# Optimization experiments

Hardware: AMD Instinct MI355X
Metric: run time of the kernel (lower is better)

The kernel has to match this reference:

```python
import jax, jax.numpy as jnp
import numpy as np

EBD_DIM = 32
N_PARTS = 17
B, P, H, W = 16, 20, 128, 128


def _gather_vecs(ebds, kpts):
    # ebds: [17*D, H, W]; kpts: [P, 17, 2] normalized coords in [0,1)
    D = EBD_DIM
    flat = ebds.reshape(N_PARTS, D, H * W).transpose(0, 2, 1)  # [17, HW, D]
    ys = jnp.floor(kpts[..., 0] * H).astype(jnp.int32)          # [P, 17]
    xs = jnp.floor(kpts[..., 1] * W).astype(jnp.int32)          # [P, 17]
    lin = ys * W + xs                                           # [P, 17]
    k = jnp.arange(N_PARTS)[None, :]                            # [1, 17] part index
    return flat[k, lin]                                         # [P, 17, D]


def setup_inputs() -> dict:
    key = jax.random.key(0)
    k1, k2 = jax.random.split(key)
    ebd_batch = jax.random.normal(k1, (B, N_PARTS * EBD_DIM, H, W), dtype=jnp.float32)
    kpts = jax.random.uniform(k2, (B, P, N_PARTS, 2), dtype=jnp.float32)
    return {"ebd_batch": ebd_batch, "kpts": kpts}


def reference(ebd_batch, kpts):
    # Gather per-keypoint embedding vectors: [B, P, 17, D]
    vecs = jax.vmap(_gather_vecs)(ebd_batch, kpts)
    # Per-person mean embedding (segment mean over the 17 keypoints): [B, P, D]
    means = vecs.mean(axis=2)
    # Pull: per person, mean |vec - person_mean| (elementwise abs, matching
    # the original sqrt(x**2)), summed over people -> [B]
    pull = jnp.abs(vecs - means[:, :, None, :]).mean(axis=(2, 3)).sum(axis=1)
    # Push: mean pairwise |mean_p - mean_q| over P x P pairs and D dims -> [B]
    push = jnp.abs(means[:, :, None, :] - means[:, None, :, :]).mean(axis=(1, 2, 3))
    return (push.mean() + pull.mean()) / 2
```

## Files before the change

### kernel.cpp

```cpp
#include <hip/hip_runtime.h>
#include <math.h>

#define BB 16
#define PP 20
#define NPARTS 17
#define DD 32
#define HH 128
#define WW 128
#define HWN (HH*WW)
#define CC (NPARTS*DD)

__device__ __forceinline__ float block_sum_256(float v, float* wsum) {
    #pragma unroll
    for (int off = 32; off > 0; off >>= 1) v += __shfl_down(v, off);
    int lane = threadIdx.x & 63;
    int wid  = threadIdx.x >> 6;
    if (lane == 0) wsum[wid] = v;
    __syncthreads();
    float t = 0.f;
    if (threadIdx.x == 0) t = wsum[0] + wsum[1] + wsum[2] + wsum[3];
    return t;
}

__global__ __launch_bounds__(256) void k1_gather_pull(
        const float* __restrict__ ebd, const float* __restrict__ kpts,
        float* __restrict__ means, float* __restrict__ pull_pp) {
    const int bp  = blockIdx.x;
    const int b   = bp / PP;
    const int tid = threadIdx.x;

    __shared__ float vec[CC];
    __shared__ int   lin[NPARTS];
    __shared__ float mean_s[DD];
    __shared__ float wsum[4];

    if (tid < NPARTS) {
        float ky = kpts[(bp * NPARTS + tid) * 2 + 0];
        float kx = kpts[(bp * NPARTS + tid) * 2 + 1];
        int y = (int)floorf(ky * (float)HH);
        int x = (int)floorf(kx * (float)WW);
        y = min(max(y, 0), HH - 1);
        x = min(max(x, 0), WW - 1);
        lin[tid] = y * WW + x;
    }
    __syncthreads();

    const float* base = ebd + (size_t)b * CC * HWN;
    for (int i = tid; i < CC; i += 256) {
        int k = i >> 5;
        vec[i] = base[(size_t)i * HWN + lin[k]];
    }
    __syncthreads();

    if (tid < DD) {
        float s = 0.f;
        #pragma unroll
        for (int k = 0; k < NPARTS; ++k) s += vec[k * DD + tid];
        float m = s * (1.0f / (float)NPARTS);
        mean_s[tid] = m;
        means[bp * DD + tid] = m;
    }
    __syncthreads();

    float ps = 0.f;
    for (int i = tid; i < CC; i += 256)
        ps += fabsf(vec[i] - mean_s[i & (DD - 1)]);

    float tot = block_sum_256(ps, wsum);
    if (tid == 0) pull_pp[bp] = tot * (1.0f / (float)CC);
}

__global__ __launch_bounds__(256) void k2_push(
        const float* __restrict__ means, float* __restrict__ push_b) {
    const int b   = blockIdx.x;
    const int tid = threadIdx.x;

    __shared__ float m[PP * DD];
    __shared__ float wsum[4];

    for (int i = tid; i < PP * DD; i += 256)
        m[i] = means[b * PP * DD + i];
    __syncthreads();

    float ps = 0.f;
    for (int i = tid; i < PP * PP * DD; i += 256) {
        int d  = i & (DD - 1);
        int pq = i >> 5;
        int p  = pq / PP;
        int q  = pq - p * PP;
        ps += fabsf(m[p * DD + d] - m[q * DD + d]);
    }

    float tot = block_sum_256(ps, wsum);
    if (tid == 0) push_b[b] = tot * (1.0f / (float)(PP * PP * DD));
}

__global__ __launch_bounds__(256) void k3_final(
        const float* __restrict__ pull_pp, const float* __restrict__ push_b,
        float* __restrict__ out) {
    const int tid = threadIdx.x;
    __shared__ float wsum[4];

    float s = 0.f;
    for (int i = tid; i < BB * PP; i += 256) s += pull_pp[i];
    if (tid < BB) s += push_b[tid];

    float tot = block_sum_256(s, wsum);
    if (tid == 0) out[0] = tot * (1.0f / (2.0f * (float)BB));
}

extern "C" void kernel_launch(void* const* d_in, const int* in_sizes, int n_in,
                              void* d_out, int out_size, void* d_ws, size_t ws_size,
                              hipStream_t stream) {
    const float* ebd  = (const float*)d_in[0];
    const float* kpts = (const float*)d_in[1];
    float* out = (float*)d_out;

    float* ws       = (float*)d_ws;
    float* means    = ws;
    float* pull_pp  = means + BB * PP * DD;
    float* push_b   = pull_pp + BB * PP;

    k1_gather_pull<<<BB * PP, 256, 0, stream>>>(ebd, kpts, means, pull_pp);
    k2_push<<<BB, 256, 0, stream>>>(means, push_b);
    k3_final<<<1, 256, 0, stream>>>(pull_pp, push_b, out);
}
```

Baseline: 16.72 us.

## Fuse final reduction into push kernel via last-block atomic counter

Merges the push and final-reduction kernels into one, so the last block to finish, detected with an atomic counter, sums per-batch partials and writes the output. This removes one kernel launch. The counter is reset inside the gather kernel. The push loop is also restructured so each of 160 threads handles one person and a float4 slice, iterating over all partners and reading LDS with vector loads. This drops the per-element integer division but leaves fewer threads active.

```diff
diff --git a/kernel.cpp b/kernel.cpp
--- a/kernel.cpp
+++ b/kernel.cpp
@@ -24,10 +24,13 @@
 
 __global__ __launch_bounds__(256) void k1_gather_pull(
         const float* __restrict__ ebd, const float* __restrict__ kpts,
-        float* __restrict__ means, float* __restrict__ pull_pp) {
+        float* __restrict__ means, float* __restrict__ pull_pp,
+        unsigned int* __restrict__ counter) {
     const int bp  = blockIdx.x;
     const int b   = bp / PP;
     const int tid = threadIdx.x;
+
+    if (bp == 0 && tid == 0) *counter = 0u;
 
     __shared__ float vec[CC];
     __shared__ int   lin[NPARTS];
@@ -70,8 +73,10 @@
     if (tid == 0) pull_pp[bp] = tot * (1.0f / (float)CC);
 }
 
-__global__ __launch_bounds__(256) void k2_push(
-        const float* __restrict__ means, float* __restrict__ push_b) {
+__global__ __launch_bounds__(256) void k2_push_final(
+        const float* __restrict__ means, const float* __restrict__ pull_pp,
+        float* __restrict__ partial_b, unsigned int* __restrict__ counter,
+        float* __restrict__ out) {
     const int b   = blockIdx.x;
     const int tid = threadIdx.x;
 
@@ -82,31 +87,37 @@
         m[i] = means[b * PP * DD + i];
     __syncthreads();
 
-    float ps = 0.f;
-    for (int i = tid; i < PP * PP * DD; i += 256) {
-        int d  = i & (DD - 1);
-        int pq = i >> 5;
-        int p  = pq / PP;
-        int q  = pq - p * PP;
-        ps += fabsf(m[p * DD + d] - m[q * DD + d]);
+    float acc = 0.f;
+    if (tid < PP * (DD / 4)) {
+        int p  = tid >> 3;
+        int d4 = tid & 7;
+        float4 mp = *reinterpret_cast<const float4*>(&m[p * DD + d4 * 4]);
+        #pragma unroll
+        for (int q = 0; q < PP; ++q) {
+            float4 mq = *reinterpret_cast<const float4*>(&m[q * DD + d4 * 4]);
+            acc += fabsf(mp.x - mq.x) + fabsf(mp.y - mq.y)
+                 + fabsf(mp.z - mq.z) + fabsf(mp.w - mq.w);
+        }
     }
+    float v = acc * (1.0f / (float)(PP * PP * DD));
+    if (tid < PP) v += pull_pp[b * PP + tid];
 
-    float tot = block_sum_256(ps, wsum);
-    if (tid == 0) push_b[b] = tot * (1.0f / (float)(PP * PP * DD));
-}
+    float tot = block_sum_256(v, wsum);
 
-__global__ __launch_bounds__(256) void k3_final(
-        const float* __restrict__ pull_pp, const float* __restrict__ push_b,
-        float* __restrict__ out) {
-    const int tid = threadIdx.x;
-    __shared__ float wsum[4];
-
-    float s = 0.f;
-    for (int i = tid; i < BB * PP; i += 256) s += pull_pp[i];
-    if (tid < BB) s += push_b[tid];
-
-    float tot = block_sum_256(s, wsum);
-    if (tid == 0) out[0] = tot * (1.0f / (2.0f * (float)BB));
+    if (tid == 0) {
+        __hip_atomic_store(&partial_b[b], tot, __ATOMIC_RELEASE,
+                           __HIP_MEMORY_SCOPE_AGENT);
+        unsigned int old = __hip_atomic_fetch_add(counter, 1u, __ATOMIC_ACQ_REL,
+                                                  __HIP_MEMORY_SCOPE_AGENT);
+        if (old == BB - 1) {
+            float s = 0.f;
+            #pragma unroll
+            for (int i = 0; i < BB; ++i)
+                s += __hip_atomic_load(&partial_b[i], __ATOMIC_ACQUIRE,
+                                       __HIP_MEMORY_SCOPE_AGENT);
+            out[0] = s * (1.0f / (2.0f * (float)BB));
+        }
+    }
 }
 
 extern "C" void kernel_launch(void* const* d_in, const int* in_sizes, int n_in,
@@ -116,12 +127,12 @@
     const float* kpts = (const float*)d_in[1];
     float* out = (float*)d_out;
 
-    float* ws       = (float*)d_ws;
-    float* means    = ws;
-    float* pull_pp  = means + BB * PP * DD;
-    float* push_b   = pull_pp + BB * PP;
+    float* ws            = (float*)d_ws;
+    float* means         = ws;
+    float* pull_pp       = means + BB * PP * DD;
+    float* partial_b     = pull_pp + BB * PP;
+    unsigned int* counter = (unsigned int*)(partial_b + BB);
 
-    k1_gather_pull<<<BB * PP, 256, 0, stream>>>(ebd, kpts, means, pull_pp);
-    k2_push<<<BB, 256, 0, stream>>>(means, push_b);
-    k3_final<<<1, 256, 0, stream>>>(pull_pp, push_b, out);
+    k1_gather_pull<<<BB * PP, 256, 0, stream>>>(ebd, kpts, means, pull_pp, counter);
+    k2_push_final<<<BB, 256, 0, stream>>>(means, pull_pp, partial_b, counter, out);
 }
```

After: 16.11 us, median of 2. 1.04x faster.
